# Optimization experiments

Measured on AMD Instinct MI355X. Metric: run time of the kernel, lower is better.

The kernel has to match this reference:

```python
import jax, jax.numpy as jnp
import numpy as np

NEG_INF = -1e9  # mask fill value used by the original layer
LEAKY_SLOPE = 0.2


def setup_inputs() -> dict:
    key = jax.random.key(0)
    k1, k2, k3, k4 = jax.random.split(key, 4)
    B, N, D_in = 8, 1024, 256
    H, head_dim = 8, 32  # output_dim=256, concat_heads=True
    node_features = jax.random.normal(k1, (B, N, D_in), dtype=jnp.float32)
    adjacency = jax.random.randint(k2, (B, N, N), 0, 2, dtype=jnp.int32)
    W = jax.random.normal(k3, (H, D_in, head_dim), dtype=jnp.float32) * (1.0 / np.sqrt(D_in))
    a = jax.random.normal(k4, (H, 2 * head_dim), dtype=jnp.float32) * (1.0 / np.sqrt(2 * head_dim))
    bias = jnp.zeros((H * head_dim,), dtype=jnp.float32)
    return {"node_features": node_features, "adjacency": adjacency, "W": W, "a": a, "bias": bias}


def reference(node_features, adjacency, W, a, bias):
    # node_features: (B,N,D_in); adjacency: (B,N,N) in {0,1}
    H, _, hd = W.shape
    # Per-head linear transform: (B,H,N,head_dim)
    Wh = jnp.einsum('bni,hij->bhnj', node_features, W)
    # a @ concat(h_i, h_j) == a1 @ h_i + a2 @ h_j  (avoids O(N^2*2hd) concat)
    a1, a2 = a[:, :hd], a[:, hd:]
    e_i = jnp.einsum('bhnj,hj->bhn', Wh, a1)  # (B,H,N) source term
    e_j = jnp.einsum('bhnj,hj->bhn', Wh, a2)  # (B,H,N) target term
    scores = e_i[:, :, :, None] + e_j[:, :, None, :]  # (B,H,N,N)
    # LeakyReLU(0.2) exactly as ops.maximum(x, 0.2*x)
    scores = jnp.maximum(scores, LEAKY_SLOPE * scores)
    mask = adjacency.astype(scores.dtype)[:, None, :, :]  # (B,1,N,N)
    masked = scores * mask + (1.0 - mask) * NEG_INF
    attn = jax.nn.softmax(masked, axis=-1)  # (B,H,N,N)
    attended = jnp.einsum('bhij,bhjk->bhik', attn, Wh)  # (B,H,N,hd)
    B, _, N, _ = attended.shape
    # concat heads -> (B,N,H*hd); head order matches the python loop concat
    out = attended.transpose(0, 2, 1, 3).reshape(B, N, H * hd)
    out = out + bias
    return jax.nn.relu(out)
```

## Files before the change

kernel.cpp:

```cpp
#include <hip/hip_runtime.h>

#define GAT_B   8
#define GAT_N   1024
#define GAT_DIN 256
#define GAT_H   8
#define GAT_HD  32
#define GAT_LOG2E 1.4426950408889634f

typedef unsigned short gu16;
typedef unsigned int   gu32;
typedef unsigned long long gu64;
typedef __bf16 bf16x8 __attribute__((ext_vector_type(8)));
typedef __bf16 bf16x4 __attribute__((ext_vector_type(4)));
typedef float  f32x4v __attribute__((ext_vector_type(4)));

#if __has_builtin(__builtin_amdgcn_exp2f)
#define GAT_EXP2(x) __builtin_amdgcn_exp2f(x)
#else
#define GAT_EXP2(x) exp2f(x)
#endif

__device__ __forceinline__ float gb2f(gu16 u) { return __uint_as_float(((gu32)u) << 16); }

__device__ __forceinline__ void gat_detect(const gu16* p, int t, int* sflag) {
    if (t < 64) {
        int e0 = (p[2 * t]     >> 7) & 0xFF;
        int e1 = (p[2 * t + 1] >> 7) & 0xFF;
        unsigned long long m = __ballot((e0 >= 140) || (e1 >= 140));
        if (t == 0) *sflag = (m != 0ULL);
    }
}

__global__ __launch_bounds__(512) void CustomGATLayer_90348932038855_pack(
    const void* __restrict__ Xv, const void* __restrict__ Wv, const void* __restrict__ biasv,
    __bf16* __restrict__ wfg, float* __restrict__ biasf)
{
    __shared__ int sflag;
    const int t = threadIdx.x, h = blockIdx.x;
    gat_detect((const gu16*)Xv, t, &sflag);
    __syncthreads();
    const int fp32 = sflag;

    if (h == 0 && t < 64) {
        if (fp32) {
            const float* bp = (const float*)biasv;
            #pragma unroll
            for (int q = 0; q < 4; ++q) biasf[t * 4 + q] = bp[t * 4 + q];
        } else {
            const gu16* bp = (const gu16*)biasv;
            #pragma unroll
            for (int q = 0; q < 4; ++q) biasf[t * 4 + q] = gb2f(bp[t * 4 + q]);
        }
    }

    if (fp32) {
        const float* ws = (const float*)Wv + (size_t)h * 8192;
        #pragma unroll
        for (int q = 0; q < 4; ++q) {
            int idx = q * 2048 + t * 4;
            int i = idx >> 5, k = idx & 31;
            float4 v = *(const float4*)(ws + idx);
            int d = h * 8192 + (((i >> 5) * 32 + k) * 4 + ((i >> 3) & 3)) * 8 + (i & 7);
            wfg[d] = (__bf16)v.x; wfg[d + 32] = (__bf16)v.y;
            wfg[d + 64] = (__bf16)v.z; wfg[d + 96] = (__bf16)v.w;
        }
    } else {
        const gu16* ws = (const gu16*)Wv + (size_t)h * 8192;
        gu16* wo = (gu16*)wfg;
        #pragma unroll
        for (int q = 0; q < 4; ++q) {
            int idx = q * 2048 + t * 4;
            int i = idx >> 5, k = idx & 31;
            ushort4 v = *(const ushort4*)(ws + idx);
            int d = h * 8192 + (((i >> 5) * 32 + k) * 4 + ((i >> 3) & 3)) * 8 + (i & 7);
            wo[d] = v.x; wo[d + 32] = v.y; wo[d + 64] = v.z; wo[d + 96] = v.w;
        }
    }
}

__global__ __launch_bounds__(512) void CustomGATLayer_90348932038855_kernel(
    const void* __restrict__ Xv, const __bf16* __restrict__ wfg, const void* __restrict__ Av,
    const int* __restrict__ adj, gu32* __restrict__ pk32,
    __bf16* __restrict__ whb, float* __restrict__ e1, float* __restrict__ e2)
{
    __shared__ __align__(16) __bf16 Xl[16][264];
    __shared__ int sflag;

    const int t = threadIdx.x;
    const int bt = blockIdx.x;
    const int M0 = bt * 16, b = M0 >> 10, nloc = M0 & 1023;

    gat_detect((const gu16*)Xv, t, &sflag);
    const int srow = t >> 5, scol = (t & 31) * 8;
    __syncthreads();
    const int fp32 = sflag;

    float4 x0, x1; bf16x8 xraw;
    if (fp32) {
        const float* xs = (const float*)Xv + ((size_t)(b * GAT_N + nloc + srow)) * GAT_DIN + scol;
        x0 = *(const float4*)(xs);
        x1 = *(const float4*)(xs + 4);
    } else {
        const gu16* xs = (const gu16*)Xv + ((size_t)(b * GAT_N + nloc + srow)) * GAT_DIN + scol;
        xraw = *(const bf16x8*)xs;
    }

    const int arow = t >> 5, adw = t & 31;
    const int* aro = adj + ((size_t)(M0 + arow)) * GAT_N + adw * 32;
    const int4 a0 = *(const int4*)(aro);      const int4 a1 = *(const int4*)(aro + 4);
    const int4 a2 = *(const int4*)(aro + 8);  const int4 a3 = *(const int4*)(aro + 12);
    const int4 a4 = *(const int4*)(aro + 16); const int4 a5 = *(const int4*)(aro + 20);
    const int4 a6 = *(const int4*)(aro + 24); const int4 a7 = *(const int4*)(aro + 28);

    if (fp32) {
        bf16x8 xv;
        xv[0] = (__bf16)x0.x; xv[1] = (__bf16)x0.y; xv[2] = (__bf16)x0.z; xv[3] = (__bf16)x0.w;
        xv[4] = (__bf16)x1.x; xv[5] = (__bf16)x1.y; xv[6] = (__bf16)x1.z; xv[7] = (__bf16)x1.w;
        *(bf16x8*)&Xl[srow][scol] = xv;
    } else {
        *(bf16x8*)&Xl[srow][scol] = xraw;
    }
    __syncthreads();

    const int h = t >> 6, l = t & 63, g = l >> 4, c = l & 15;
    const __bf16* wf = wfg + h * 8192;

    f32x4v acc0 = {0.f, 0.f, 0.f, 0.f};
    f32x4v acc1 = {0.f, 0.f, 0.f, 0.f};
    #pragma unroll
    for (int kc = 0; kc < 8; ++kc) {
        bf16x8 af = *(const bf16x8*)&Xl[c][kc * 32 + 8 * g];
        bf16x8 b0 = *(const bf16x8*)(wf + ((kc * 32 + c) * 4 + g) * 8);
        bf16x8 b1 = *(const bf16x8*)(wf + ((kc * 32 + c + 16) * 4 + g) * 8);
        acc0 = __builtin_amdgcn_mfma_f32_16x16x32_bf16(af, b0, acc0, 0, 0, 0);
        acc1 = __builtin_amdgcn_mfma_f32_16x16x32_bf16(af, b1, acc1, 0, 0, 0);
    }

    const int nb = nloc + 4 * g;
    const int jcc = nb >> 5, kg = (nb >> 3) & 3, e0 = nb & 7;
    const size_t fb = (((size_t)(b * GAT_H + h) * 32 + jcc) * 4 + kg) * 32;
    bf16x4 v0, v1;
    v0[0] = (__bf16)acc0[0]; v0[1] = (__bf16)acc0[1];
    v0[2] = (__bf16)acc0[2]; v0[3] = (__bf16)acc0[3];
    v1[0] = (__bf16)acc1[0]; v1[1] = (__bf16)acc1[1];
    v1[2] = (__bf16)acc1[2]; v1[3] = (__bf16)acc1[3];
    *(bf16x4*)(whb + (fb + c) * 8 + e0)      = v0;
    *(bf16x4*)(whb + (fb + c + 16) * 8 + e0) = v1;

    float a1c, a1c16, a2c, a2c16;
    if (fp32) {
        const float* ap = (const float*)Av + h * 2 * GAT_HD;
        a1c = ap[c] * GAT_LOG2E;      a1c16 = ap[c + 16] * GAT_LOG2E;
        a2c = ap[32 + c] * GAT_LOG2E; a2c16 = ap[48 + c] * GAT_LOG2E;
    } else {
        const gu16* ap = (const gu16*)Av + h * 2 * GAT_HD;
        a1c = gb2f(ap[c]) * GAT_LOG2E;      a1c16 = gb2f(ap[c + 16]) * GAT_LOG2E;
        a2c = gb2f(ap[32 + c]) * GAT_LOG2E; a2c16 = gb2f(ap[48 + c]) * GAT_LOG2E;
    }
    float p1[4], p2[4];
    #pragma unroll
    for (int q = 0; q < 4; ++q) {
        p1[q] = acc0[q] * a1c + acc1[q] * a1c16;
        p2[q] = acc0[q] * a2c + acc1[q] * a2c16;
        #pragma unroll
        for (int mm = 1; mm <= 8; mm <<= 1) {
            p1[q] += __shfl_xor(p1[q], mm);
            p2[q] += __shfl_xor(p2[q], mm);
        }
    }
    if (c == 0) {
        const size_t eb = (size_t)(b * GAT_H + h) * GAT_N + nb;
        #pragma unroll
        for (int q = 0; q < 4; ++q) { e1[eb + q] = p1[q]; e2[eb + q] = p2[q]; }
    }

    gu32 m = 0;
    m |= (a0.x != 0 ? 1u : 0u)       | (a0.y != 0 ? 2u : 0u)
       | (a0.z != 0 ? 4u : 0u)       | (a0.w != 0 ? 8u : 0u);
    m |= (a1.x != 0 ? 16u : 0u)      | (a1.y != 0 ? 32u : 0u)
       | (a1.z != 0 ? 64u : 0u)      | (a1.w != 0 ? 128u : 0u);
    m |= (a2.x != 0 ? 256u : 0u)     | (a2.y != 0 ? 512u : 0u)
       | (a2.z != 0 ? 1024u : 0u)    | (a2.w != 0 ? 2048u : 0u);
    m |= (a3.x != 0 ? 4096u : 0u)    | (a3.y != 0 ? 8192u : 0u)
       | (a3.z != 0 ? 16384u : 0u)   | (a3.w != 0 ? 32768u : 0u);
    m |= (a4.x != 0 ? 1u << 16 : 0u) | (a4.y != 0 ? 1u << 17 : 0u)
       | (a4.z != 0 ? 1u << 18 : 0u) | (a4.w != 0 ? 1u << 19 : 0u);
    m |= (a5.x != 0 ? 1u << 20 : 0u) | (a5.y != 0 ? 1u << 21 : 0u)
       | (a5.z != 0 ? 1u << 22 : 0u) | (a5.w != 0 ? 1u << 23 : 0u);
    m |= (a6.x != 0 ? 1u << 24 : 0u) | (a6.y != 0 ? 1u << 25 : 0u)
       | (a6.z != 0 ? 1u << 26 : 0u) | (a6.w != 0 ? 1u << 27 : 0u);
    m |= (a7.x != 0 ? 1u << 28 : 0u) | (a7.y != 0 ? 1u << 29 : 0u)
       | (a7.z != 0 ? 1u << 30 : 0u) | (a7.w != 0 ? 1u << 31 : 0u);
    pk32[((size_t)(M0 + arow)) * 32 + adw] = m;
}

__global__ __launch_bounds__(1024, 8) void CustomGATLayer_90348932038855_attn(
    const gu32* __restrict__ pk32, const float* __restrict__ biasf,
    const __bf16* __restrict__ whb, const float* __restrict__ e1f, const float* __restrict__ e2f,
    float* __restrict__ out)
{
    __shared__ __align__(16) float e2l[GAT_H][1024];
    __shared__ gu32 pkl[16][33];

    const int t = threadIdx.x;
    const int w = t >> 6, l = t & 63, g = l >> 4, c = l & 15;
    const int h = w & 7, jh = w >> 3;
    const int id = blockIdx.x;
    const int b = id & 7, tile = id >> 3;
    const int i0 = tile * 16;

    if (t < 512) {
        pkl[t >> 5][t & 31] = pk32[((size_t)(b * GAT_N + i0 + (t >> 5))) * 32 + (t & 31)];
    }
    {
        const float* s = e2f + (size_t)(b * GAT_H + h) * GAT_N + jh * 512;
        float* d = &e2l[h][jh * 512];
        #pragma unroll
        for (int q = 0; q < 2; ++q) {
            int off = (q * 64 + l) * 4;
            *(float4*)(d + off) = *(const float4*)(s + off);
        }
    }
    __syncthreads();

    const float e1r = e1f[(size_t)(b * GAT_H + h) * GAT_N + i0 + c];
    const __bf16* whr = whb + (size_t)(b * GAT_H + h) * (GAT_N * GAT_HD)
                            + jh * 16384 + g * 256 + c * 8;
    const float* e2h = &e2l[h][jh * 512 + 8 * g];
    const gu32* pkr = &pkl[c][jh * 16];

    bf16x8 wA0 = *(const bf16x8*)(whr),        wA1 = *(const bf16x8*)(whr + 128);
    bf16x8 wB0 = *(const bf16x8*)(whr + 1024), wB1 = *(const bf16x8*)(whr + 1152);
    bf16x8 wC0 = *(const bf16x8*)(whr + 2048), wC1 = *(const bf16x8*)(whr + 2176);

    f32x4v acc0 = {0.f, 0.f, 0.f, 0.f};
    f32x4v acc1 = {0.f, 0.f, 0.f, 0.f};
    f32x4v accS = {0.f, 0.f, 0.f, 0.f};
    bf16x8 onesf;
    #pragma unroll
    for (int e = 0; e < 8; ++e) onesf[e] = (__bf16)1.0f;

#define GAT_WCOMP(EV, IDX) {                        \
        float s_ = e1r + (EV);                      \
        s_ = fmaxf(s_, 0.2f * s_);                  \
        float w_ = GAT_EXP2(s_);                    \
        w_ = (ab & (1u << IDX)) ? w_ : 0.0f;        \
        pf[IDX] = (__bf16)w_; }

    #pragma unroll 2
    for (int jc = 0; jc < 16; ++jc) {
        const bf16x8 w0 = wA0, w1 = wA1;
        wA0 = wB0; wA1 = wB1; wB0 = wC0; wB1 = wC1;
        if (jc < 13) {
            const __bf16* wn = whr + (jc + 3) * 1024;
            wC0 = *(const bf16x8*)wn; wC1 = *(const bf16x8*)(wn + 128);
        }
        const gu32 ab = (pkr[jc] >> (8 * g)) & 0xFFu;
        float4 ea = *(const float4*)(e2h + jc * 32);
        float4 eb = *(const float4*)(e2h + jc * 32 + 4);
        bf16x8 pf;
        GAT_WCOMP(ea.x, 0) GAT_WCOMP(ea.y, 1)
        GAT_WCOMP(ea.z, 2) GAT_WCOMP(ea.w, 3)
        GAT_WCOMP(eb.x, 4) GAT_WCOMP(eb.y, 5)
        GAT_WCOMP(eb.z, 6) GAT_WCOMP(eb.w, 7)
        acc0 = __builtin_amdgcn_mfma_f32_16x16x32_bf16(pf, w0, acc0, 0, 0, 0);
        acc1 = __builtin_amdgcn_mfma_f32_16x16x32_bf16(pf, w1, acc1, 0, 0, 0);
        accS = __builtin_amdgcn_mfma_f32_16x16x32_bf16(pf, onesf, accS, 0, 0, 0);
    }
#undef GAT_WCOMP

    __syncthreads();
    float4* sc = (float4*)e2l;
    const int slot = h * 64 + l;
    if (jh == 1) {
        sc[slot]        = make_float4(acc0[0], acc0[1], acc0[2], acc0[3]);
        sc[512 + slot]  = make_float4(acc1[0], acc1[1], acc1[2], acc1[3]);
        sc[1024 + slot] = make_float4(accS[0], accS[1], accS[2], accS[3]);
    }
    __syncthreads();
    if (jh == 0) {
        float4 q0 = sc[slot], q1 = sc[512 + slot], q2 = sc[1024 + slot];
        acc0[0] += q0.x; acc0[1] += q0.y; acc0[2] += q0.z; acc0[3] += q0.w;
        acc1[0] += q1.x; acc1[1] += q1.y; acc1[2] += q1.z; acc1[3] += q1.w;
        accS[0] += q2.x; accS[1] += q2.y; accS[2] += q2.z; accS[3] += q2.w;

        const float bv0 = biasf[h * GAT_HD + c];
        const float bv1 = biasf[h * GAT_HD + c + 16];

        float* ob = out + (size_t)(b * GAT_N + i0) * (GAT_H * GAT_HD) + h * GAT_HD + c;
        #pragma unroll
        for (int q = 0; q < 4; ++q) {
            float d = accS[q];
            float r = (d > 0.f) ? (1.0f / d) : 0.0f;
            float o0 = fmaxf(acc0[q] * r + bv0, 0.f);
            float o1 = fmaxf(acc1[q] * r + bv1, 0.f);
            ob[(size_t)(4 * g + q) * (GAT_H * GAT_HD)]      = o0;
            ob[(size_t)(4 * g + q) * (GAT_H * GAT_HD) + 16] = o1;
        }
    }
}

extern "C" void kernel_launch(void* const* d_in, const int* in_sizes, int n_in,
                              void* d_out, int out_size, void* d_ws, size_t ws_size,
                              hipStream_t stream) {
    const void* X    = d_in[0];
    const int*  adj  = (const int*)d_in[1];
    const void* Wm   = d_in[2];
    const void* Av   = d_in[3];
    const void* bias = d_in[4];
    float* outp = (float*)d_out;

    __bf16* whb = (__bf16*)d_ws;
    float* e1   = (float*)(whb + (size_t)GAT_B * GAT_H * GAT_N * GAT_HD);
    float* e2   = e1 + (size_t)GAT_B * GAT_H * GAT_N;
    __bf16* wfg = (__bf16*)(e2 + (size_t)GAT_B * GAT_H * GAT_N);
    gu32* pk32  = (gu32*)(wfg + (size_t)GAT_H * GAT_DIN * GAT_HD);
    float* biasf = (float*)(pk32 + (size_t)GAT_B * GAT_N * 32);

    CustomGATLayer_90348932038855_pack
        <<<dim3(8), 512, 0, stream>>>(X, Wm, bias, wfg, biasf);
    CustomGATLayer_90348932038855_kernel
        <<<dim3(512), 512, 0, stream>>>(X, wfg, Av, adj, pk32, whb, e1, e2);
    CustomGATLayer_90348932038855_attn
        <<<dim3((GAT_N / 16) * GAT_B), 1024, 0, stream>>>(
            pk32, biasf, whb, e1, e2, outp);
}
```

Baseline: 124.9 us.

## Stage per-head Wh in LDS and split attention blocks by head and row group

The attention kernel is reorganised so each block handles one (batch, head) pair and 64 query rows, instead of 16 rows across all heads. The block first copies that head's whole Wh slice (64 KB bf16) into LDS, and its 16 waves share it across 4 row tiles and 4 column quarters. This cuts repeated global/L2 reads of Wh, which the old layout re-fetched for every 16-row tile. The cost is more LDS per block, which may lower occupancy, plus a 4-way cross-wave reduction in place of the old 2-way one.

```diff
diff --git a/kernel.cpp b/kernel.cpp
--- a/kernel.cpp
+++ b/kernel.cpp
@@ -199,39 +199,39 @@
     const __bf16* __restrict__ whb, const float* __restrict__ e1f, const float* __restrict__ e2f,
     float* __restrict__ out)
 {
-    __shared__ __align__(16) float e2l[GAT_H][1024];
-    __shared__ gu32 pkl[16][33];
+    __shared__ __align__(16) __bf16 whl[32768];
+    __shared__ gu32 pkl[64][33];
+    __shared__ __align__(16) float e2l[GAT_N];
 
     const int t = threadIdx.x;
     const int w = t >> 6, l = t & 63, g = l >> 4, c = l & 15;
-    const int h = w & 7, jh = w >> 3;
+    const int rt = w >> 2, jq = w & 3;
     const int id = blockIdx.x;
-    const int b = id & 7, tile = id >> 3;
-    const int i0 = tile * 16;
-
-    if (t < 512) {
-        pkl[t >> 5][t & 31] = pk32[((size_t)(b * GAT_N + i0 + (t >> 5))) * 32 + (t & 31)];
-    }
+    const int b = id & 7, h = (id >> 3) & 7, rg = id >> 6;
+    const int i0 = rg * 64;
+    const int bh = b * GAT_H + h;
+
     {
-        const float* s = e2f + (size_t)(b * GAT_H + h) * GAT_N + jh * 512;
-        float* d = &e2l[h][jh * 512];
-        #pragma unroll
-        for (int q = 0; q < 2; ++q) {
-            int off = (q * 64 + l) * 4;
-            *(float4*)(d + off) = *(const float4*)(s + off);
-        }
-    }
-    __syncthreads();
-
-    const float e1r = e1f[(size_t)(b * GAT_H + h) * GAT_N + i0 + c];
-    const __bf16* whr = whb + (size_t)(b * GAT_H + h) * (GAT_N * GAT_HD)
-                            + jh * 16384 + g * 256 + c * 8;
-    const float* e2h = &e2l[h][jh * 512 + 8 * g];
-    const gu32* pkr = &pkl[c][jh * 16];
-
-    bf16x8 wA0 = *(const bf16x8*)(whr),        wA1 = *(const bf16x8*)(whr + 128);
-    bf16x8 wB0 = *(const bf16x8*)(whr + 1024), wB1 = *(const bf16x8*)(whr + 1152);
-    bf16x8 wC0 = *(const bf16x8*)(whr + 2048), wC1 = *(const bf16x8*)(whr + 2176);
+        const bf16x8* src = (const bf16x8*)(whb + (size_t)bh * (GAT_N * GAT_HD));
+        bf16x8* dst = (bf16x8*)whl;
+        #pragma unroll
+        for (int q = 0; q < 4; ++q) dst[q * 1024 + t] = src[q * 1024 + t];
+    }
+    #pragma unroll
+    for (int q = 0; q < 2; ++q) {
+        int idx = q * 1024 + t;
+        int r = idx >> 5, d = idx & 31;
+        pkl[r][d] = pk32[((size_t)(b * GAT_N + i0 + r)) * 32 + d];
+    }
+    if (t < 256) {
+        ((float4*)e2l)[t] = ((const float4*)(e2f + (size_t)bh * GAT_N))[t];
+    }
+    const float e1r = e1f[(size_t)bh * GAT_N + i0 + rt * 16 + c];
+    __syncthreads();
+
+    const gu32*  pkr = &pkl[rt * 16 + c][jq * 8];
+    const float* e2h = e2l + jq * 256 + 8 * g;
+    const __bf16* whr = whl + jq * 8192 + g * 256 + c * 8;
 
     f32x4v acc0 = {0.f, 0.f, 0.f, 0.f};
     f32x4v acc1 = {0.f, 0.f, 0.f, 0.f};
@@ -248,13 +248,9 @@
         pf[IDX] = (__bf16)w_; }
 
     #pragma unroll 2
-    for (int jc = 0; jc < 16; ++jc) {
-        const bf16x8 w0 = wA0, w1 = wA1;
-        wA0 = wB0; wA1 = wB1; wB0 = wC0; wB1 = wC1;
-        if (jc < 13) {
-            const __bf16* wn = whr + (jc + 3) * 1024;
-            wC0 = *(const bf16x8*)wn; wC1 = *(const bf16x8*)(wn + 128);
-        }
+    for (int jc = 0; jc < 8; ++jc) {
+        const bf16x8 w0 = *(const bf16x8*)(whr + jc * 1024);
+        const bf16x8 w1 = *(const bf16x8*)(whr + jc * 1024 + 128);
         const gu32 ab = (pkr[jc] >> (8 * g)) & 0xFFu;
         float4 ea = *(const float4*)(e2h + jc * 32);
         float4 eb = *(const float4*)(e2h + jc * 32 + 4);
@@ -270,24 +266,29 @@
 #undef GAT_WCOMP
 
     __syncthreads();
-    float4* sc = (float4*)e2l;
-    const int slot = h * 64 + l;
-    if (jh == 1) {
+    float4* sc = (float4*)whl;
+    const int slot = (rt * 4 + jq) * 64 + l;
+    if (jq != 0) {
         sc[slot]        = make_float4(acc0[0], acc0[1], acc0[2], acc0[3]);
-        sc[512 + slot]  = make_float4(acc1[0], acc1[1], acc1[2], acc1[3]);
-        sc[1024 + slot] = make_float4(accS[0], accS[1], accS[2], accS[3]);
-    }
-    __syncthreads();
-    if (jh == 0) {
-        float4 q0 = sc[slot], q1 = sc[512 + slot], q2 = sc[1024 + slot];
-        acc0[0] += q0.x; acc0[1] += q0.y; acc0[2] += q0.z; acc0[3] += q0.w;
-        acc1[0] += q1.x; acc1[1] += q1.y; acc1[2] += q1.z; acc1[3] += q1.w;
-        accS[0] += q2.x; accS[1] += q2.y; accS[2] += q2.z; accS[3] += q2.w;
+        sc[1024 + slot] = make_float4(acc1[0], acc1[1], acc1[2], acc1[3]);
+        sc[2048 + slot] = make_float4(accS[0], accS[1], accS[2], accS[3]);
+    }
+    __syncthreads();
+    if (jq == 0) {
+        #pragma unroll
+        for (int p = 1; p < 4; ++p) {
+            const int s2 = (rt * 4 + p) * 64 + l;
+            float4 q0 = sc[s2], q1 = sc[1024 + s2], q2 = sc[2048 + s2];
+            acc0[0] += q0.x; acc0[1] += q0.y; acc0[2] += q0.z; acc0[3] += q0.w;
+            acc1[0] += q1.x; acc1[1] += q1.y; acc1[2] += q1.z; acc1[3] += q1.w;
+            accS[0] += q2.x; accS[1] += q2.y; accS[2] += q2.z; accS[3] += q2.w;
+        }
 
         const float bv0 = biasf[h * GAT_HD + c];
         const float bv1 = biasf[h * GAT_HD + c + 16];
 
-        float* ob = out + (size_t)(b * GAT_N + i0) * (GAT_H * GAT_HD) + h * GAT_HD + c;
+        float* ob = out + (size_t)(b * GAT_N + i0 + rt * 16) * (GAT_H * GAT_HD)
+                        + h * GAT_HD + c;
         #pragma unroll
         for (int q = 0; q < 4; ++q) {
             float d = accS[q];
@@ -322,6 +323,6 @@
     CustomGATLayer_90348932038855_kernel
         <<<dim3(512), 512, 0, stream>>>(X, wfg, Av, adj, pk32, whb, e1, e2);
     CustomGATLayer_90348932038855_attn
-        <<<dim3((GAT_N / 16) * GAT_B), 1024, 0, stream>>>(
+        <<<dim3(16 * GAT_H * GAT_B), 1024, 0, stream>>>(
             pk32, biasf, whb, e1, e2, outp);
 }
```

After: 121.2 us. -3.0%, faster.
